# Kernel tuning notes

Hardware: AMD Instinct MI355X
Metric: run time of the kernel (lower is better)

Reference implementation:

```python
import jax, jax.numpy as jnp
import numpy as np

# HGT meta: 2 node types (A=0, B=1), 3 relations (src_type, dst_type)
L, T, R = 3, 2, 3
H, D = 1, 64            # PyG HGTConv default heads=1, head_dim = hidden/heads
F = H * D               # hidden_channels = input feature dim = 64
NA = NB = 131072
E = 1_000_000
REL = [(0, 1), (1, 0), (0, 0)]


def setup_inputs() -> dict:
    key = jax.random.key(0)
    ks = jax.random.split(key, 16)
    sc = 1.0 / np.sqrt(F)
    inp = {}
    inp["xA"] = jax.random.normal(ks[0], (NA, F), jnp.float32)
    inp["xB"] = jax.random.normal(ks[1], (NB, F), jnp.float32)
    # K/Q/V projections per (layer, node_type)
    inp["Wk"] = jax.random.normal(ks[2], (L, T, F, F), jnp.float32) * sc
    inp["bk"] = jnp.zeros((L, T, F), jnp.float32)
    inp["Wq"] = jax.random.normal(ks[3], (L, T, F, F), jnp.float32) * sc
    inp["bq"] = jnp.zeros((L, T, F), jnp.float32)
    inp["Wv"] = jax.random.normal(ks[4], (L, T, F, F), jnp.float32) * sc
    inp["bv"] = jnp.zeros((L, T, F), jnp.float32)
    # per (layer, relation, head) attention / message matrices and priority
    inp["a_rel"] = jax.random.normal(ks[5], (L, R, H, D, D), jnp.float32) * sc
    inp["m_rel"] = jax.random.normal(ks[6], (L, R, H, D, D), jnp.float32) * sc
    inp["p_rel"] = jnp.ones((L, R, H), jnp.float32)
    # output projection + skip gate per (layer, node_type)
    inp["Wa"] = jax.random.normal(ks[7], (L, T, F, F), jnp.float32) * sc
    inp["ba"] = jnp.zeros((L, T, F), jnp.float32)
    inp["skip"] = jnp.ones((L, T), jnp.float32)
    # final readout Linear(hidden, 1)
    inp["lin_w"] = jax.random.normal(ks[8], (F, 1), jnp.float32) * sc
    inp["lin_b"] = jnp.zeros((1,), jnp.float32)
    # edge indices: ei[0]=src, ei[1]=dst (NA == NB so one range works)
    inp["ei1"] = jax.random.randint(ks[9], (2, E), 0, NA, jnp.int32)   # A -> B
    inp["ei2"] = jax.random.randint(ks[10], (2, E), 0, NA, jnp.int32)  # B -> A
    inp["ei3"] = jax.random.randint(ks[11], (2, E), 0, NA, jnp.int32)  # A -> A
    return inp


def _hgt_layer(xs, eis, Wk, bk, Wq, bq, Wv, bv, a_rel, m_rel, p_rel, Wa, ba, skip):
    # per-type K/Q/V projections, reshaped to [N, H, D]
    k = [(xs[t] @ Wk[t] + bk[t]).reshape(-1, H, D) for t in range(T)]
    q = [(xs[t] @ Wq[t] + bq[t]).reshape(-1, H, D) for t in range(T)]
    v = [(xs[t] @ Wv[t] + bv[t]).reshape(-1, H, D) for t in range(T)]
    agg = [jnp.zeros((xs[t].shape[0], H, D), xs[t].dtype) for t in range(T)]
    inv_sqrt_d = jnp.asarray(1.0 / np.sqrt(D), xs[0].dtype)
    for r, (s, d) in enumerate(REL):
        src, dst = eis[r][0], eis[r][1]
        n_d = xs[d].shape[0]
        # relation-specific transforms on source nodes, then edge gather
        k_r = jnp.einsum('nhd,hde->nhe', k[s], a_rel[r])
        v_r = jnp.einsum('nhd,hde->nhe', v[s], m_rel[r])
        # attention score per edge per head: (q_dst . k_src) * p_rel / sqrt(D)
        score = jnp.einsum('ehd,ehd->eh', q[d][dst], k_r[src]) * p_rel[r] * inv_sqrt_d
        # segment softmax over incoming edges of each dst node (per edge type)
        mx = jax.ops.segment_max(score, dst, num_segments=n_d)
        ex = jnp.exp(score - mx[dst])
        den = jax.ops.segment_sum(ex, dst, num_segments=n_d)
        alpha = ex / den[dst]                      # [E, H]
        msg = alpha[:, :, None] * v_r[src]         # [E, H, D]
        agg[d] = agg[d] + jax.ops.segment_sum(msg, dst, num_segments=n_d)
    outs = []
    for t in range(T):
        o = jax.nn.gelu(agg[t].reshape(-1, F), approximate=False) @ Wa[t] + ba[t]
        a = jax.nn.sigmoid(skip[t])               # skip gate (out_dim == in_dim)
        outs.append(a * o + (1.0 - a) * xs[t])
    return outs


def reference(xA, xB, Wk, bk, Wq, bq, Wv, bv, a_rel, m_rel, p_rel, Wa, ba, skip,
              lin_w, lin_b, ei1, ei2, ei3):
    xs = [xA, xB]
    eis = [ei1, ei2, ei3]
    for l in range(L):
        xs = _hgt_layer(xs, eis, Wk[l], bk[l], Wq[l], bq[l], Wv[l], bv[l],
                        a_rel[l], m_rel[l], p_rel[l], Wa[l], ba[l], skip[l])
    x = jnp.concatenate(xs, axis=0)               # concat all node types
    pooled = jnp.sum(x, axis=0, keepdims=True)    # global_add_pool, batch=None
    return pooled @ lin_w + lin_b                 # Linear(hidden, 1) -> [1, 1]
```

## Files before the change

### kernel.cpp

```cpp
#include <hip/hip_runtime.h>
#include <cmath>

#define DEV __device__ __forceinline__

typedef __attribute__((ext_vector_type(8))) short short8v;
typedef __attribute__((ext_vector_type(4))) float f32x4;

DEV float atomicAddF(float* p, float v) {
    return unsafeAtomicAdd(p, v);
}

DEV float gelu_exact(float v) {
    return 0.5f * v * (1.f + erff(v * 0.70710678118654752f));
}

DEV unsigned short f32_to_bf16(float f) {
    union { float f; unsigned int u; } x; x.f = f;
    unsigned int r = x.u + 0x7fffu + ((x.u >> 16) & 1u);
    return (unsigned short)(r >> 16);
}

DEV unsigned int f4_to_fp8x4(float a, float b, float c, float d) {
    int r = __builtin_amdgcn_cvt_pk_fp8_f32(a, b, 0, false);
    r = __builtin_amdgcn_cvt_pk_fp8_f32(c, d, r, true);
    return (unsigned int)r;
}

DEV float4 fp8x4_to_f4(unsigned int w) {
    auto lo = __builtin_amdgcn_cvt_pk_f32_fp8(w, false);
    auto hi = __builtin_amdgcn_cvt_pk_f32_fp8(w, true);
    return make_float4(lo[0], lo[1], hi[0], hi[1]);
}

DEV short8v cvt8_bf16(float4 f0, float4 f1) {
    union { unsigned int u[4]; short8v s; } r;
    asm("v_cvt_pk_bf16_f32 %0, %1, %2" : "=v"(r.u[0]) : "v"(f0.x), "v"(f0.y));
    asm("v_cvt_pk_bf16_f32 %0, %1, %2" : "=v"(r.u[1]) : "v"(f0.z), "v"(f0.w));
    asm("v_cvt_pk_bf16_f32 %0, %1, %2" : "=v"(r.u[2]) : "v"(f1.x), "v"(f1.y));
    asm("v_cvt_pk_bf16_f32 %0, %1, %2" : "=v"(r.u[3]) : "v"(f1.z), "v"(f1.w));
    return r.s;
}


struct MatSetB {
    const unsigned short* Wt[3];
    const float* b[3];
    float*       y[3];
    int          mode[3];
    int          n;
};

#define BCAP2 4608
#define SB_TILE 4096
#define PSTR 129

__global__ __launch_bounds__(256) void combine_w_bf16(
    const float* __restrict__ Wk, const float* __restrict__ bk,
    const float* __restrict__ Wv, const float* __restrict__ bv,
    const float* __restrict__ a_rel, const float* __restrict__ m_rel,
    const float* __restrict__ p_rel, unsigned short* __restrict__ CWt,
    float* __restrict__ Cb)
{
    const int r = blockIdx.x, kv = blockIdx.y, l = blockIdx.z;
    const int srcT[3] = {0, 1, 0};
    const int s = srcT[r];
    const float* Wsrc = (kv == 0 ? Wk : Wv) + ((size_t)(l*2 + s)) * 4096;
    const float* bsrc = (kv == 0 ? bk : bv) + ((size_t)(l*2 + s)) * 64;
    const float* A    = (kv == 0 ? a_rel : m_rel) + ((size_t)(l*3 + r)) * 4096;
    const float scale = (kv == 0) ? p_rel[l*3 + r] * 0.125f : 1.f;

    __shared__ float Ws[4096];
    __shared__ float As[4096];
    const int tid = threadIdx.x;
    for (int k = tid; k < 4096; k += 256) { Ws[k] = Wsrc[k]; As[k] = A[k]; }
    __syncthreads();

    unsigned short* out = CWt + ((size_t)(l*6 + r*2 + kv)) * 4096;
    const int j = tid & 63;
    #pragma unroll
    for (int i = 0; i < 16; i++) {
        const int f = (tid >> 6) * 16 + i;
        float acc = 0.f;
        #pragma unroll
        for (int e = 0; e < 64; e++) acc = fmaf(Ws[f*64 + e], As[e*64 + j], acc);
        const int so = (l == 0) ? f : (4*(f & 15) + (f >> 4));
        out[j*64 + so] = f32_to_bf16(acc * scale);
    }
    if (tid < 64) {
        float acc = 0.f;
        for (int e = 0; e < 64; e++) acc = fmaf(bsrc[e], As[e*64 + tid], acc);
        Cb[(size_t)(l*6 + r*2 + kv) * 64 + tid] = acc * scale;
    }
}

__global__ __launch_bounds__(256) void prep_wt(
    const float* __restrict__ Wq, const float* __restrict__ Wa,
    unsigned short* __restrict__ Wqt, unsigned short* __restrict__ Wat)
{
    const int bid = blockIdx.x;
    const float* src; unsigned short* dst; int useSigma;
    if (bid < 6) { src = Wq + (size_t)bid * 4096; dst = Wqt + (size_t)bid * 4096;
                   useSigma = (bid >= 2); }
    else         { src = Wa + (size_t)(bid - 6) * 4096; dst = Wat + (size_t)(bid - 6) * 4096;
                   useSigma = 1; }
    for (int idx = threadIdx.x; idx < 4096; idx += 256) {
        const int c = idx >> 6, s = idx & 63;
        const int k = useSigma ? (16*(s & 3) + (s >> 2)) : s;
        dst[c*64 + s] = f32_to_bf16(src[k*64 + c]);
    }
}

DEV void proj128_body(const float* __restrict__ x, const MatSetB& ms, int bid, int tid)
{
    const int wv  = tid >> 6;
    const int ln  = tid & 63;
    const int j   = ln & 15;
    const int g   = ln >> 4;
    const long long rowb = (long long)bid * 128 + wv * 32;

    short8v A[2][2];
    #pragma unroll
    for (int rg = 0; rg < 2; rg++) {
        const float* xp = x + (rowb + rg*16 + j) * 64 + g*8;
        #pragma unroll
        for (int ks = 0; ks < 2; ks++) {
            const float4 f0 = *(const float4*)(xp + ks*32);
            const float4 f1 = *(const float4*)(xp + ks*32 + 4);
            A[rg][ks] = cvt8_bf16(f0, f1);
        }
    }

    unsigned int kst[2][4];
    for (int m = 0; m < ms.n; m++) {
        short8v B[4][2];
        #pragma unroll
        for (int ct = 0; ct < 4; ct++) {
            const unsigned short* wp = ms.Wt[m] + (ct*16 + j) * 64 + g*8;
            B[ct][0] = *(const short8v*)(wp);
            B[ct][1] = *(const short8v*)(wp + 32);
        }
        f32x4 acc[2][4];
        #pragma unroll
        for (int ct = 0; ct < 4; ct++) {
            const float bm = ms.b[m][ct*16 + j];
            f32x4 bi = {bm, bm, bm, bm};
            acc[0][ct] = bi; acc[1][ct] = bi;
        }
        #pragma unroll
        for (int rg = 0; rg < 2; rg++)
            #pragma unroll
            for (int ct = 0; ct < 4; ct++) {
                acc[rg][ct] = __builtin_amdgcn_mfma_f32_16x16x32_bf16(
                    A[rg][0], B[ct][0], acc[rg][ct], 0, 0, 0);
                acc[rg][ct] = __builtin_amdgcn_mfma_f32_16x16x32_bf16(
                    A[rg][1], B[ct][1], acc[rg][ct], 0, 0, 0);
            }
        const int mode = ms.mode[m];
        if (mode == 0) {
            float* yb = ms.y[m];
            #pragma unroll
            for (int rg = 0; rg < 2; rg++)
                #pragma unroll
                for (int i = 0; i < 4; i++) {
                    const long long node = rowb + rg*16 + g*4 + i;
                    *(float4*)(yb + node*64 + j*4) = make_float4(
                        acc[rg][0][i], acc[rg][1][i], acc[rg][2][i], acc[rg][3][i]);
                }
        } else if (mode == 1) {
            #pragma unroll
            for (int rg = 0; rg < 2; rg++)
                #pragma unroll
                for (int i = 0; i < 4; i++)
                    kst[rg][i] = f4_to_fp8x4(
                        acc[rg][0][i], acc[rg][1][i], acc[rg][2][i], acc[rg][3][i]);
        } else {
            unsigned char* yb = (unsigned char*)ms.y[m];
            #pragma unroll
            for (int rg = 0; rg < 2; rg++)
                #pragma unroll
                for (int i = 0; i < 4; i++) {
                    const long long node = rowb + rg*16 + g*4 + i;
                    uint2 s;
                    s.x = kst[rg][i];
                    s.y = f4_to_fp8x4(
                        acc[rg][0][i], acc[rg][1][i], acc[rg][2][i], acc[rg][3][i]);
                    *(uint2*)(yb + node*128 + j*8) = s;
                }
        }
    }
}

__global__ __launch_bounds__(256) void proj_triple(
    const float* __restrict__ x1, MatSetB ms1, int g1,
    const float* __restrict__ x2, MatSetB ms2, int g2,
    const float* __restrict__ x3, MatSetB ms3)
{
    const int tid = threadIdx.x;
    int idx = blockIdx.x;
    if (idx < g1) { proj128_body(x1, ms1, idx, tid); return; }
    idx -= g1;
    if (idx < g2) { proj128_body(x2, ms2, idx, tid); return; }
    proj128_body(x3, ms3, idx - g2, tid);
}

struct ScatP { const int* ei; int E; int nbuck; int* bcur; int2* pb; int nblk; };

DEV void scatter_body(const ScatP& sp, int bid, int tid)
{
    __shared__ int  hist[256];
    __shared__ int  lbase[256];
    __shared__ int  gbase[256];
    __shared__ int  lcur[256];
    __shared__ int  scanbuf[256];
    __shared__ int2 stage[SB_TILE];
    const int tile0 = bid * SB_TILE;
    const int E = sp.E;
    const int* ei = sp.ei;

    int2 my[16]; int mb[16];
    #pragma unroll
    for (int i = 0; i < 16; i++) {
        const int e = tile0 + tid + i*256;
        if (e < E) { my[i].x = ei[e]; my[i].y = ei[E + e]; mb[i] = my[i].y >> 9; }
        else mb[i] = -1;
    }
    hist[tid] = 0;
    __syncthreads();
    #pragma unroll
    for (int i = 0; i < 16; i++) if (mb[i] >= 0) atomicAdd(&hist[mb[i]], 1);
    __syncthreads();
    const int c = hist[tid];
    scanbuf[tid] = c;
    __syncthreads();
    for (int off = 1; off < 256; off <<= 1) {
        int add = (tid >= off) ? scanbuf[tid - off] : 0;
        __syncthreads();
        scanbuf[tid] += add;
        __syncthreads();
    }
    lbase[tid] = scanbuf[tid] - c;
    lcur[tid]  = scanbuf[tid] - c;
    if (c > 0 && tid < sp.nbuck) gbase[tid] = atomicAdd(sp.bcur + tid * 16, c);
    __syncthreads();
    #pragma unroll
    for (int i = 0; i < 16; i++) {
        if (mb[i] >= 0) {
            const int p = atomicAdd(&lcur[mb[i]], 1);
            stage[p] = my[i];
        }
    }
    __syncthreads();
    if (c > 0 && tid < sp.nbuck) {
        const int gb = gbase[tid];
        const int lb = lbase[tid];
        int2* dstp = sp.pb + (size_t)tid * BCAP2;
        for (int jj = 0; jj < c; jj++) {
            const int gp = gb + jj;
            if (gp < BCAP2) dstp[gp] = stage[lb + jj];
        }
    }
}

__global__ __launch_bounds__(256) void proj_scatter(
    ScatP s0, ScatP s1, ScatP s2,
    const float* __restrict__ x1, MatSetB ms1, int g1,
    const float* __restrict__ x2, MatSetB ms2, int g2,
    const float* __restrict__ x3, MatSetB ms3)
{
    const int tid = threadIdx.x;
    int idx = blockIdx.x;
    if (idx < s0.nblk) { scatter_body(s0, idx, tid); return; }
    idx -= s0.nblk;
    if (idx < s1.nblk) { scatter_body(s1, idx, tid); return; }
    idx -= s1.nblk;
    if (idx < s2.nblk) { scatter_body(s2, idx, tid); return; }
    idx -= s2.nblk;
    if (idx < g1) { proj128_body(x1, ms1, idx, tid); return; }
    idx -= g1;
    if (idx < g2) { proj128_body(x2, ms2, idx, tid); return; }
    proj128_body(x3, ms3, idx - g2, tid);
}

struct CsrP { const int2* pb; const int* bcur; int* rp; int* re; int* col; int n; int nblk; };

DEV void csr_body(const CsrP& cp, int b, int tid)
{
    __shared__ int lcnt[512];
    __shared__ int lcur[512];
    __shared__ int scanbuf[256];
    int cnt = cp.bcur[b * 16];
    if (cnt > BCAP2) cnt = BCAP2;
    lcnt[tid] = 0; lcnt[tid + 256] = 0;
    __syncthreads();
    const int2* src = cp.pb + (size_t)b * BCAP2;
    for (int i = tid; i < cnt; i += 256)
        atomicAdd(&lcnt[src[i].y & 511], 1);
    __syncthreads();
    const int c0 = lcnt[2*tid], c1 = lcnt[2*tid + 1];
    const int s = c0 + c1;
    scanbuf[tid] = s;
    __syncthreads();
    for (int off = 1; off < 256; off <<= 1) {
        int add = (tid >= off) ? scanbuf[tid - off] : 0;
        __syncthreads();
        scanbuf[tid] += add;
        __syncthreads();
    }
    const int excl = scanbuf[tid] - s;
    const int base = b * BCAP2;
    const int d0 = (b << 9) + 2*tid;
    if (d0 < cp.n)     { cp.rp[d0]   = base + excl;      cp.re[d0]   = base + excl + c0; }
    if (d0 + 1 < cp.n) { cp.rp[d0+1] = base + excl + c0; cp.re[d0+1] = base + excl + c0 + c1; }
    lcur[2*tid] = excl; lcur[2*tid + 1] = excl + c0;
    __syncthreads();
    for (int i = tid; i < cnt; i += 256) {
        const int2 p = src[i];
        const int pos = atomicAdd(&lcur[p.y & 511], 1);
        cp.col[base + pos] = p.x;
    }
}

__global__ __launch_bounds__(256) void csr_all(CsrP c0, CsrP c1, CsrP c2)
{
    const int tid = threadIdx.x;
    int idx = blockIdx.x;
    if (idx < c0.nblk) { csr_body(c0, idx, tid); return; }
    idx -= c0.nblk;
    if (idx < c1.nblk) { csr_body(c1, idx, tid); return; }
    csr_body(c2, idx - c1.nblk, tid);
}

#define PROC_EDGE(KVR)                                                                 \
    {                                                                                  \
        const float4 ka_ = fp8x4_to_f4(KVR.x);                                         \
        const float4 kb2_ = fp8x4_to_f4(KVR.z);                                        \
        float sc_ = q0.x*ka_.x + q0.y*ka_.y + q0.z*ka_.z + q0.w*ka_.w                  \
                  + q1.x*kb2_.x + q1.y*kb2_.y + q1.z*kb2_.z + q1.w*kb2_.w;             \
        sc_ += __shfl_xor(sc_, 1); sc_ += __shfl_xor(sc_, 2); sc_ += __shfl_xor(sc_, 4);\
        const float p_ = __expf(sc_);                                                  \
        const float4 va_ = fp8x4_to_f4(KVR.y);                                         \
        const float4 vb_ = fp8x4_to_f4(KVR.w);                                         \
        ssum_ += p_;                                                                   \
        acc0_.x = fmaf(p_, va_.x, acc0_.x); acc0_.y = fmaf(p_, va_.y, acc0_.y);        \
        acc0_.z = fmaf(p_, va_.z, acc0_.z); acc0_.w = fmaf(p_, va_.w, acc0_.w);        \
        acc1_.x = fmaf(p_, vb_.x, acc1_.x); acc1_.y = fmaf(p_, vb_.y, acc1_.y);        \
        acc1_.z = fmaf(p_, vb_.z, acc1_.z); acc1_.w = fmaf(p_, vb_.w, acc1_.w);        \
    }

#define AGG_BODY(RP, RE, COL, KV, O0, O1)                                              \
    {                                                                                  \
        float4 acc0_ = {0.f,0.f,0.f,0.f}, acc1_ = {0.f,0.f,0.f,0.f};                   \
        float ssum_ = 0.f;                                                             \
        const int ss0_ = (RP)[dst], ss1_ = (RE)[dst];                                  \
        const unsigned char* kb_ = (KV) + sub*16;                                      \
        int e_ = ss0_;                                                                 \
        uint4 qq0_ = {0,0,0,0}, qq1_ = {0,0,0,0}, qq2_ = {0,0,0,0}, qq3_ = {0,0,0,0};  \
        if (e_ < ss1_)     qq0_ = *(const uint4*)(kb_ + (size_t)(COL)[e_] * 128);      \
        if (e_ + 1 < ss1_) qq1_ = *(const uint4*)(kb_ + (size_t)(COL)[e_+1] * 128);    \
        if (e_ + 2 < ss1_) qq2_ = *(const uint4*)(kb_ + (size_t)(COL)[e_+2] * 128);    \
        if (e_ + 3 < ss1_) qq3_ = *(const uint4*)(kb_ + (size_t)(COL)[e_+3] * 128);    \
        for (; e_ + 4 < ss1_; e_ += 2) {                                               \
            const int nn0_ = (COL)[e_+4];                                              \
            const int nn1_ = (e_ + 5 < ss1_) ? (COL)[e_+5] : nn0_;                     \
            const uint4 tt0_ = *(const uint4*)(kb_ + (size_t)nn0_ * 128);              \
            const uint4 tt1_ = *(const uint4*)(kb_ + (size_t)nn1_ * 128);              \
            PROC_EDGE(qq0_)                                                            \
            PROC_EDGE(qq1_)                                                            \
            qq0_ = qq2_; qq1_ = qq3_; qq2_ = tt0_; qq3_ = tt1_;                        \
        }                                                                              \
        if (e_ < ss1_)     PROC_EDGE(qq0_)                                             \
        if (e_ + 1 < ss1_) PROC_EDGE(qq1_)                                             \
        if (e_ + 2 < ss1_) PROC_EDGE(qq2_)                                             \
        if (e_ + 3 < ss1_) PROC_EDGE(qq3_)                                             \
        const float inv_ = (ssum_ > 0.f) ? 1.f / ssum_ : 0.f;                          \
        O0.x = fmaf(acc0_.x, inv_, O0.x); O0.y = fmaf(acc0_.y, inv_, O0.y);            \
        O0.z = fmaf(acc0_.z, inv_, O0.z); O0.w = fmaf(acc0_.w, inv_, O0.w);            \
        O1.x = fmaf(acc1_.x, inv_, O1.x); O1.y = fmaf(acc1_.y, inv_, O1.y);            \
        O1.z = fmaf(acc1_.z, inv_, O1.z); O1.w = fmaf(acc1_.w, inv_, O1.w);            \
    }

DEV void agg_block(
    const int* __restrict__ rp1, const int* __restrict__ re1, const int* __restrict__ c1,
    const int* __restrict__ rp2, const int* __restrict__ re2, const int* __restrict__ c2,
    const float* __restrict__ q,
    const unsigned char* __restrict__ kva, const unsigned char* __restrict__ kvb,
    float* __restrict__ xio, const unsigned short* __restrict__ Wat,
    const float* __restrict__ ba, const float* __restrict__ skipw,
    int xstd, int dual, int dopool, float* __restrict__ vec,
    int bid, int tid, float* lds, float* lds_pool)
{
    const long long rowb = (long long)bid * 128;
    if (tid < 64) lds_pool[tid] = 0.f;

    {
        const int sub = tid & 7;
        const int dl  = tid >> 3;
        const int dst = (int)rowb + dl;
        const float4* qp = (const float4*)(q + (size_t)dst * 64);
        const float4 q0 = qp[sub*2], q1 = qp[sub*2 + 1];
        float4 o0 = {0.f,0.f,0.f,0.f}, o1 = {0.f,0.f,0.f,0.f};
        AGG_BODY(rp1, re1, c1, kva, o0, o1)
        if (dual) {
            AGG_BODY(rp2, re2, c2, kvb, o0, o1)
        }
        float* lp = lds + (size_t)(8*sub) * PSTR + dl;
        lp[0*PSTR] = gelu_exact(o0.x); lp[1*PSTR] = gelu_exact(o0.y);
        lp[2*PSTR] = gelu_exact(o0.z); lp[3*PSTR] = gelu_exact(o0.w);
        lp[4*PSTR] = gelu_exact(o1.x); lp[5*PSTR] = gelu_exact(o1.y);
        lp[6*PSTR] = gelu_exact(o1.z); lp[7*PSTR] = gelu_exact(o1.w);
    }
    __syncthreads();

    if (tid < 512) {
        const int wv = tid >> 6;
        const int ln = tid & 63;
        const int j  = ln & 15;
        const int g  = ln >> 4;
        const int r  = wv*16 + j;

        short8v A[2];
        #pragma unroll
        for (int ks = 0; ks < 2; ks++) {
            const int pb = g*8 + ks*32;
            const float4 f0 = make_float4(lds[(pb+0)*PSTR + r], lds[(pb+1)*PSTR + r],
                                          lds[(pb+2)*PSTR + r], lds[(pb+3)*PSTR + r]);
            const float4 f1 = make_float4(lds[(pb+4)*PSTR + r], lds[(pb+5)*PSTR + r],
                                          lds[(pb+6)*PSTR + r], lds[(pb+7)*PSTR + r]);
            A[ks] = cvt8_bf16(f0, f1);
        }

        f32x4 acc[4];
        #pragma unroll
        for (int ct = 0; ct < 4; ct++) {
            const float bm = ba[ct*16 + j];
            acc[ct] = (f32x4){bm, bm, bm, bm};
        }
        #pragma unroll
        for (int ct = 0; ct < 4; ct++) {
            const unsigned short* wp = Wat + (ct*16 + j) * 64 + g*8;
            const short8v B0 = *(const short8v*)(wp);
            const short8v B1 = *(const short8v*)(wp + 32);
            acc[ct] = __builtin_amdgcn_mfma_f32_16x16x32_bf16(A[0], B0, acc[ct], 0, 0, 0);
            acc[ct] = __builtin_amdgcn_mfma_f32_16x16x32_bf16(A[1], B1, acc[ct], 0, 0, 0);
        }

        const float gate = 1.f / (1.f + __expf(-skipw[0]));
        const float og   = 1.f - gate;
        float4 pacc = {0.f,0.f,0.f,0.f};
        #pragma unroll
        for (int i = 0; i < 4; i++) {
            const long long node = rowb + wv*16 + g*4 + i;
            float* xp = xio + node*64;
            float4 o;
            if (xstd) {
                o.x = gate*acc[0][i] + og*xp[j];
                o.y = gate*acc[1][i] + og*xp[16 + j];
                o.z = gate*acc[2][i] + og*xp[32 + j];
                o.w = gate*acc[3][i] + og*xp[48 + j];
            } else {
                const float4 xo = *(const float4*)(xp + 4*j);
                o = make_float4(gate*acc[0][i] + og*xo.x,
                                gate*acc[1][i] + og*xo.y,
                                gate*acc[2][i] + og*xo.z,
                                gate*acc[3][i] + og*xo.w);
            }
            if (!dopool) {
                *(float4*)(xp + 4*j) = o;
            } else {
                pacc.x += o.x; pacc.y += o.y; pacc.z += o.z; pacc.w += o.w;
            }
        }
        if (dopool) {
            atomicAdd(&lds_pool[4*j + 0], pacc.x);
            atomicAdd(&lds_pool[4*j + 1], pacc.y);
            atomicAdd(&lds_pool[4*j + 2], pacc.z);
            atomicAdd(&lds_pool[4*j + 3], pacc.w);
        }
    }
    __syncthreads();
    if (dopool && tid < 64) atomicAddF(vec + tid, lds_pool[tid]);
}

__global__ __launch_bounds__(1024, 8) void agg_all(
    const int* __restrict__ rp0, const int* __restrict__ re0, const int* __restrict__ c0,
    const float* __restrict__ qB, const unsigned char* __restrict__ kv0,
    float* __restrict__ xB, const unsigned short* __restrict__ WatB,
    const float* __restrict__ baB, const float* __restrict__ skipB,
    const int* __restrict__ rp1, const int* __restrict__ re1, const int* __restrict__ c1,
    const int* __restrict__ rp2, const int* __restrict__ re2, const int* __restrict__ c2,
    const float* __restrict__ qA, const unsigned char* __restrict__ kv1,
    const unsigned char* __restrict__ kv2,
    float* __restrict__ xA, const unsigned short* __restrict__ WatA,
    const float* __restrict__ baA, const float* __restrict__ skipA,
    int xstd, int dopool, float* __restrict__ vec, int aggB, int aggA)
{
    __shared__ float lds[64 * PSTR];
    __shared__ float lds_pool[64];
    const int idx = blockIdx.x;
    const int tid = threadIdx.x;
    const int half = (aggA < aggB) ? aggA : aggB;
    int isDual, bid;
    if (idx < 2*half) { isDual = !(idx & 1); bid = idx >> 1; }
    else              { bid = idx - half;    isDual = (aggA > aggB); }
    if (isDual) {
        agg_block(rp1, re1, c1, rp2, re2, c2, qA, kv1, kv2, xA, WatA, baA, skipA,
                  xstd, 1, dopool, vec, bid, tid, lds, lds_pool);
    } else {
        agg_block(rp0, re0, c0, rp0, re0, c0, qB, kv0, kv0, xB, WatB, baB, skipB,
                  xstd, 0, dopool, vec, bid, tid, lds, lds_pool);
    }
}

__global__ void final_dot(const float* __restrict__ vec, const float* __restrict__ lw,
                          const float* __restrict__ lb, float* __restrict__ out)
{
    const int i = threadIdx.x;
    float v = vec[i] * lw[16*(i & 3) + (i >> 2)];
    #pragma unroll
    for (int m = 32; m >= 1; m >>= 1) v += __shfl_xor(v, m);
    if (i == 0) out[0] = v + lb[0];
}

extern "C" void kernel_launch(void* const* d_in, const int* in_sizes, int n_in,
                              void* d_out, int out_size, void* d_ws, size_t ws_size,
                              hipStream_t stream)
{
    float* xs[2] = {(float*)d_in[0], (float*)d_in[1]};
    const float* Wk    = (const float*)d_in[2];
    const float* bk    = (const float*)d_in[3];
    const float* Wq    = (const float*)d_in[4];
    const float* bq    = (const float*)d_in[5];
    const float* Wv    = (const float*)d_in[6];
    const float* bv    = (const float*)d_in[7];
    const float* a_rel = (const float*)d_in[8];
    const float* m_rel = (const float*)d_in[9];
    const float* p_rel = (const float*)d_in[10];
    const float* Wa    = (const float*)d_in[11];
    const float* ba    = (const float*)d_in[12];
    const float* skipw = (const float*)d_in[13];
    const float* lin_w = (const float*)d_in[14];
    const float* lin_b = (const float*)d_in[15];
    const int*   ei[3] = {(const int*)d_in[16], (const int*)d_in[17], (const int*)d_in[18]};

    const long long NA = in_sizes[0] / 64;
    const long long NB = in_sizes[1] / 64;
    const long long Ns[2] = {NA, NB};
    const long long Nmax = NA > NB ? NA : NB;
    int E[3];
    for (int r = 0; r < 3; r++) E[r] = in_sizes[16 + r] / 2;
    static const int dstN_is_B[3] = {1, 0, 0};
    const long long nbuckMax = (Nmax + 511) >> 9;

    float* w = (float*)d_ws;
    float* qB  = w; w += Nmax * 64;
    float* qA  = w; w += Nmax * 64;
    unsigned char* kv0 = (unsigned char*)w; w += Nmax * 32;
    unsigned char* kv1 = (unsigned char*)w; w += Nmax * 32;
    unsigned char* kv2 = (unsigned char*)w; w += Nmax * 32;
    unsigned short* CWt = (unsigned short*)w; w += 18 * 2048;
    unsigned short* Wqt = (unsigned short*)w; w += 6 * 2048;
    unsigned short* Wat = (unsigned short*)w; w += 6 * 2048;
    float* Cb    = w; w += 18 * 64;
    float* vec   = w; w += 64;
    int* iw = (int*)w;
    int* row_ptr[3]; int* row_end[3]; int* col[3];
    for (int r = 0; r < 3; r++) {
        row_ptr[r] = iw; iw += Nmax;
        row_end[r] = iw; iw += Nmax;
        col[r]     = iw; iw += nbuckMax * BCAP2;
    }
    int* bcur_all = iw; iw += 3 * nbuckMax * 16;
    int2* pb_all  = (int2*)iw;

    combine_w_bf16<<<dim3(3, 2, 3), 256, 0, stream>>>(Wk, bk, Wv, bv, a_rel, m_rel, p_rel, CWt, Cb);
    prep_wt<<<12, 256, 0, stream>>>(Wq, Wa, Wqt, Wat);
    hipMemsetAsync(vec, 0, 64 * sizeof(float), stream);
    hipMemsetAsync(bcur_all, 0, (size_t)3 * nbuckMax * 16 * sizeof(int), stream);

    const int gA = (int)(NA >> 7), gB = (int)(NB >> 7);
    const int aggB = (int)(NB >> 7);
    const int aggA = (int)(NA >> 7);

    MatSetB msB[3], msA[3], msA2[3];
    for (int l = 0; l < 3; l++) {
        msB[l].n = 3;
        msB[l].Wt[0] = Wqt + (size_t)(l*2 + 1) * 4096;  msB[l].b[0] = bq + (size_t)(l*2 + 1) * 64;
        msB[l].y[0] = qB;         msB[l].mode[0] = 0;
        msB[l].Wt[1] = CWt + (size_t)(l*6 + 2) * 4096;  msB[l].b[1] = Cb + (size_t)(l*6 + 2) * 64;
        msB[l].y[1] = nullptr;    msB[l].mode[1] = 1;
        msB[l].Wt[2] = CWt + (size_t)(l*6 + 3) * 4096;  msB[l].b[2] = Cb + (size_t)(l*6 + 3) * 64;
        msB[l].y[2] = (float*)kv1; msB[l].mode[2] = 2;
        msA[l].n = 2;
        msA[l].Wt[0] = CWt + (size_t)(l*6 + 0) * 4096;  msA[l].b[0] = Cb + (size_t)(l*6 + 0) * 64;
        msA[l].y[0] = nullptr;    msA[l].mode[0] = 1;
        msA[l].Wt[1] = CWt + (size_t)(l*6 + 1) * 4096;  msA[l].b[1] = Cb + (size_t)(l*6 + 1) * 64;
        msA[l].y[1] = (float*)kv0; msA[l].mode[1] = 2;
        msA[l].Wt[2] = msA[l].Wt[1]; msA[l].b[2] = msA[l].b[1];
        msA[l].y[2] = msA[l].y[1];  msA[l].mode[2] = 2;
        msA2[l].n = 3;
        msA2[l].Wt[0] = Wqt + (size_t)(l*2 + 0) * 4096;  msA2[l].b[0] = bq + (size_t)(l*2 + 0) * 64;
        msA2[l].y[0] = qA;         msA2[l].mode[0] = 0;
        msA2[l].Wt[1] = CWt + (size_t)(l*6 + 4) * 4096;  msA2[l].b[1] = Cb + (size_t)(l*6 + 4) * 64;
        msA2[l].y[1] = nullptr;    msA2[l].mode[1] = 1;
        msA2[l].Wt[2] = CWt + (size_t)(l*6 + 5) * 4096;  msA2[l].b[2] = Cb + (size_t)(l*6 + 5) * 64;
        msA2[l].y[2] = (float*)kv2; msA2[l].mode[2] = 2;
    }

    ScatP sp[3];
    for (int r = 0; r < 3; r++) {
        sp[r].ei    = ei[r];
        sp[r].E     = E[r];
        sp[r].nbuck = (int)((Ns[dstN_is_B[r]] + 511) >> 9);
        sp[r].bcur  = bcur_all + (size_t)r * nbuckMax * 16;
        sp[r].pb    = pb_all + (size_t)r * nbuckMax * BCAP2;
        sp[r].nblk  = (E[r] + SB_TILE - 1) / SB_TILE;
    }
    proj_scatter<<<sp[0].nblk + sp[1].nblk + sp[2].nblk + gB + gA + gA, 256, 0, stream>>>(
        sp[0], sp[1], sp[2],
        xs[1], msB[0], gB, xs[0], msA[0], gA, xs[0], msA2[0]);

    CsrP cp[3];
    for (int r = 0; r < 3; r++) {
        cp[r].pb   = sp[r].pb;
        cp[r].bcur = sp[r].bcur;
        cp[r].rp   = row_ptr[r];
        cp[r].re   = row_end[r];
        cp[r].col  = col[r];
        cp[r].n    = (int)Ns[dstN_is_B[r]];
        cp[r].nblk = sp[r].nbuck;
    }
    csr_all<<<cp[0].nblk + cp[1].nblk + cp[2].nblk, 256, 0, stream>>>(cp[0], cp[1], cp[2]);

    for (int l = 0; l < 3; l++) {
        const int xstd   = (l == 0) ? 1 : 0;
        const int dopool = (l == 2) ? 1 : 0;
        if (l > 0) {
            proj_triple<<<gB + gA + gA, 256, 0, stream>>>(
                xs[1], msB[l], gB, xs[0], msA[l], gA, xs[0], msA2[l]);
        }
        agg_all<<<aggB + aggA, 1024, 0, stream>>>(
            row_ptr[0], row_end[0], col[0], qB, kv0, xs[1],
            Wat + (size_t)(l*2 + 1) * 4096, ba + (size_t)(l*2 + 1) * 64, skipw + l*2 + 1,
            row_ptr[1], row_end[1], col[1],
            row_ptr[2], row_end[2], col[2],
            qA, kv1, kv2, xs[0],
            Wat + (size_t)(l*2 + 0) * 4096, ba + (size_t)(l*2 + 0) * 64, skipw + l*2 + 0,
            xstd, dopool, vec, aggB, aggA);
    }

    final_dot<<<1, 64, 0, stream>>>(vec, lin_w, lin_b, (float*)d_out);
}
```

Baseline: 762.8 us.

## Fuse next-layer projections into aggregation kernel and store activations in bf16

Removes the separate per-layer proj_triple launch. Each aggregation block now keeps its updated node features in shared memory and immediately computes the next layer's Q/K/V projections with MFMA. K/V buffers are double-buffered across layers so the next layer's outputs do not overwrite data other blocks still read. Q and the intermediate node features are stored as bf16 instead of fp32, which halves their memory traffic but lowers precision. The extra shared memory and work per block may reduce occupancy of the already heavy aggregation kernel.

```diff
diff --git a/kernel.cpp b/kernel.cpp
--- a/kernel.cpp
+++ b/kernel.cpp
@@ -41,6 +41,20 @@
     return r.s;
 }
 
+DEV uint2 f4_to_bf4(float4 v) {
+    uint2 r;
+    asm("v_cvt_pk_bf16_f32 %0, %1, %2" : "=v"(r.x) : "v"(v.x), "v"(v.y));
+    asm("v_cvt_pk_bf16_f32 %0, %1, %2" : "=v"(r.y) : "v"(v.z), "v"(v.w));
+    return r;
+}
+
+DEV float4 bf4_to_f4(uint2 w) {
+    union { unsigned int u; float f; } a, b, c, d;
+    a.u = (w.x & 0xffffu) << 16; b.u =  w.x & 0xffff0000u;
+    c.u = (w.y & 0xffffu) << 16; d.u =  w.y & 0xffff0000u;
+    return make_float4(a.f, b.f, c.f, d.f);
+}
+
 
 struct MatSetB {
     const unsigned short* Wt[3];
@@ -53,6 +67,7 @@
 #define BCAP2 4608
 #define SB_TILE 4096
 #define PSTR 129
+#define XSTR 72
 
 __global__ __launch_bounds__(256) void combine_w_bf16(
     const float* __restrict__ Wk, const float* __restrict__ bk,
@@ -110,7 +125,7 @@
     }
 }
 
-DEV void proj128_body(const float* __restrict__ x, const MatSetB& ms, int bid, int tid)
+DEV void proj128_f32(const float* __restrict__ x, const MatSetB& ms, int bid, int tid)
 {
     const int wv  = tid >> 6;
     const int ln  = tid & 63;
@@ -157,14 +172,14 @@
             }
         const int mode = ms.mode[m];
         if (mode == 0) {
-            float* yb = ms.y[m];
+            unsigned short* yb = (unsigned short*)ms.y[m];
             #pragma unroll
             for (int rg = 0; rg < 2; rg++)
                 #pragma unroll
                 for (int i = 0; i < 4; i++) {
                     const long long node = rowb + rg*16 + g*4 + i;
-                    *(float4*)(yb + node*64 + j*4) = make_float4(
-                        acc[rg][0][i], acc[rg][1][i], acc[rg][2][i], acc[rg][3][i]);
+                    *(uint2*)(yb + node*64 + j*4) = f4_to_bf4(make_float4(
+                        acc[rg][0][i], acc[rg][1][i], acc[rg][2][i], acc[rg][3][i]));
                 }
         } else if (mode == 1) {
             #pragma unroll
@@ -190,17 +205,50 @@
     }
 }
 
-__global__ __launch_bounds__(256) void proj_triple(
-    const float* __restrict__ x1, MatSetB ms1, int g1,
-    const float* __restrict__ x2, MatSetB ms2, int g2,
-    const float* __restrict__ x3, MatSetB ms3)
-{
-    const int tid = threadIdx.x;
-    int idx = blockIdx.x;
-    if (idx < g1) { proj128_body(x1, ms1, idx, tid); return; }
-    idx -= g1;
-    if (idx < g2) { proj128_body(x2, ms2, idx, tid); return; }
-    proj128_body(x3, ms3, idx - g2, tid);
+DEV void run_matsets(short8v A0, short8v A1, const MatSetB& ms, int m0, int m1,
+                     long long rowt, int j, int g)
+{
+    unsigned int kst[4];
+    for (int m = m0; m < m1; m++) {
+        f32x4 acc[4];
+        #pragma unroll
+        for (int ct = 0; ct < 4; ct++) {
+            const float bm = ms.b[m][ct*16 + j];
+            acc[ct] = (f32x4){bm, bm, bm, bm};
+        }
+        #pragma unroll
+        for (int ct = 0; ct < 4; ct++) {
+            const unsigned short* wp = ms.Wt[m] + (ct*16 + j) * 64 + g*8;
+            const short8v B0 = *(const short8v*)(wp);
+            const short8v B1 = *(const short8v*)(wp + 32);
+            acc[ct] = __builtin_amdgcn_mfma_f32_16x16x32_bf16(A0, B0, acc[ct], 0, 0, 0);
+            acc[ct] = __builtin_amdgcn_mfma_f32_16x16x32_bf16(A1, B1, acc[ct], 0, 0, 0);
+        }
+        const int mode = ms.mode[m];
+        if (mode == 0) {
+            unsigned short* yb = (unsigned short*)ms.y[m];
+            #pragma unroll
+            for (int i = 0; i < 4; i++) {
+                const long long node = rowt + g*4 + i;
+                *(uint2*)(yb + node*64 + j*4) = f4_to_bf4(make_float4(
+                    acc[0][i], acc[1][i], acc[2][i], acc[3][i]));
+            }
+        } else if (mode == 1) {
+            #pragma unroll
+            for (int i = 0; i < 4; i++)
+                kst[i] = f4_to_fp8x4(acc[0][i], acc[1][i], acc[2][i], acc[3][i]);
+        } else {
+            unsigned char* yb = (unsigned char*)ms.y[m];
+            #pragma unroll
+            for (int i = 0; i < 4; i++) {
+                const long long node = rowt + g*4 + i;
+                uint2 s;
+                s.x = kst[i];
+                s.y = f4_to_fp8x4(acc[0][i], acc[1][i], acc[2][i], acc[3][i]);
+                *(uint2*)(yb + node*128 + j*8) = s;
+            }
+        }
+    }
 }
 
 struct ScatP { const int* ei; int E; int nbuck; int* bcur; int2* pb; int nblk; };
@@ -275,10 +323,10 @@
     idx -= s1.nblk;
     if (idx < s2.nblk) { scatter_body(s2, idx, tid); return; }
     idx -= s2.nblk;
-    if (idx < g1) { proj128_body(x1, ms1, idx, tid); return; }
+    if (idx < g1) { proj128_f32(x1, ms1, idx, tid); return; }
     idx -= g1;
-    if (idx < g2) { proj128_body(x2, ms2, idx, tid); return; }
-    proj128_body(x3, ms3, idx - g2, tid);
+    if (idx < g2) { proj128_f32(x2, ms2, idx, tid); return; }
+    proj128_f32(x3, ms3, idx - g2, tid);
 }
 
 struct CsrP { const int2* pb; const int* bcur; int* rp; int* re; int* col; int n; int nblk; };
@@ -382,12 +430,13 @@
 DEV void agg_block(
     const int* __restrict__ rp1, const int* __restrict__ re1, const int* __restrict__ c1,
     const int* __restrict__ rp2, const int* __restrict__ re2, const int* __restrict__ c2,
-    const float* __restrict__ q,
+    const unsigned short* __restrict__ q,
     const unsigned char* __restrict__ kva, const unsigned char* __restrict__ kvb,
-    float* __restrict__ xio, const unsigned short* __restrict__ Wat,
+    const float* __restrict__ xf, unsigned short* __restrict__ xw,
+    const unsigned short* __restrict__ Wat,
     const float* __restrict__ ba, const float* __restrict__ skipw,
     int xstd, int dual, int dopool, float* __restrict__ vec,
-    int bid, int tid, float* lds, float* lds_pool)
+    int bid, int tid, float* lds, float* lds_pool, unsigned short* xsh)
 {
     const long long rowb = (long long)bid * 128;
     if (tid < 64) lds_pool[tid] = 0.f;
@@ -396,8 +445,9 @@
         const int sub = tid & 7;
         const int dl  = tid >> 3;
         const int dst = (int)rowb + dl;
-        const float4* qp = (const float4*)(q + (size_t)dst * 64);
-        const float4 q0 = qp[sub*2], q1 = qp[sub*2 + 1];
+        const uint4 qv = *(const uint4*)(q + (size_t)dst * 64 + sub*8);
+        const float4 q0 = bf4_to_f4(make_uint2(qv.x, qv.y));
+        const float4 q1 = bf4_to_f4(make_uint2(qv.z, qv.w));
         float4 o0 = {0.f,0.f,0.f,0.f}, o1 = {0.f,0.f,0.f,0.f};
         AGG_BODY(rp1, re1, c1, kva, o0, o1)
         if (dual) {
@@ -450,22 +500,25 @@
         #pragma unroll
         for (int i = 0; i < 4; i++) {
             const long long node = rowb + wv*16 + g*4 + i;
-            float* xp = xio + node*64;
             float4 o;
             if (xstd) {
+                const float* xp = xf + node*64;
                 o.x = gate*acc[0][i] + og*xp[j];
                 o.y = gate*acc[1][i] + og*xp[16 + j];
                 o.z = gate*acc[2][i] + og*xp[32 + j];
                 o.w = gate*acc[3][i] + og*xp[48 + j];
             } else {
-                const float4 xo = *(const float4*)(xp + 4*j);
+                const float4 xo = bf4_to_f4(*(const uint2*)(xw + node*64 + 4*j));
                 o = make_float4(gate*acc[0][i] + og*xo.x,
                                 gate*acc[1][i] + og*xo.y,
                                 gate*acc[2][i] + og*xo.z,
                                 gate*acc[3][i] + og*xo.w);
             }
             if (!dopool) {
-                *(float4*)(xp + 4*j) = o;
+                const uint2 ob = f4_to_bf4(o);
+                *(uint2*)(xw + node*64 + 4*j) = ob;
+                if (xsh)
+                    *(uint2*)(xsh + (size_t)(wv*16 + g*4 + i) * XSTR + 4*j) = ob;
             } else {
                 pacc.x += o.x; pacc.y += o.y; pacc.z += o.z; pacc.w += o.w;
             }
@@ -483,31 +536,53 @@
 
 __global__ __launch_bounds__(1024, 8) void agg_all(
     const int* __restrict__ rp0, const int* __restrict__ re0, const int* __restrict__ c0,
-    const float* __restrict__ qB, const unsigned char* __restrict__ kv0,
-    float* __restrict__ xB, const unsigned short* __restrict__ WatB,
+    const unsigned short* __restrict__ qB, const unsigned char* __restrict__ kv0,
+    const float* __restrict__ xfB, unsigned short* __restrict__ xwB,
+    const unsigned short* __restrict__ WatB,
     const float* __restrict__ baB, const float* __restrict__ skipB,
     const int* __restrict__ rp1, const int* __restrict__ re1, const int* __restrict__ c1,
     const int* __restrict__ rp2, const int* __restrict__ re2, const int* __restrict__ c2,
-    const float* __restrict__ qA, const unsigned char* __restrict__ kv1,
+    const unsigned short* __restrict__ qA, const unsigned char* __restrict__ kv1,
     const unsigned char* __restrict__ kv2,
-    float* __restrict__ xA, const unsigned short* __restrict__ WatA,
+    const float* __restrict__ xfA, unsigned short* __restrict__ xwA,
+    const unsigned short* __restrict__ WatA,
     const float* __restrict__ baA, const float* __restrict__ skipA,
-    int xstd, int dopool, float* __restrict__ vec, int aggB, int aggA)
+    int xstd, int dopool, float* __restrict__ vec, int aggB, int aggA,
+    int hasNext, MatSetB msBn, MatSetB msAn, MatSetB msA2n)
 {
     __shared__ float lds[64 * PSTR];
     __shared__ float lds_pool[64];
+    __shared__ unsigned short xsh[128 * XSTR];
     const int idx = blockIdx.x;
     const int tid = threadIdx.x;
     const int half = (aggA < aggB) ? aggA : aggB;
     int isDual, bid;
     if (idx < 2*half) { isDual = !(idx & 1); bid = idx >> 1; }
     else              { bid = idx - half;    isDual = (aggA > aggB); }
+    unsigned short* xshp = hasNext ? xsh : nullptr;
     if (isDual) {
-        agg_block(rp1, re1, c1, rp2, re2, c2, qA, kv1, kv2, xA, WatA, baA, skipA,
-                  xstd, 1, dopool, vec, bid, tid, lds, lds_pool);
+        agg_block(rp1, re1, c1, rp2, re2, c2, qA, kv1, kv2, xfA, xwA, WatA, baA, skipA,
+                  xstd, 1, dopool, vec, bid, tid, lds, lds_pool, xshp);
     } else {
-        agg_block(rp0, re0, c0, rp0, re0, c0, qB, kv0, kv0, xB, WatB, baB, skipB,
-                  xstd, 0, dopool, vec, bid, tid, lds, lds_pool);
+        agg_block(rp0, re0, c0, rp0, re0, c0, qB, kv0, kv0, xfB, xwB, WatB, baB, skipB,
+                  xstd, 0, dopool, vec, bid, tid, lds, lds_pool, xshp);
+    }
+    if (!hasNext) return;
+    const int pw  = tid >> 6;
+    const int ln  = tid & 63;
+    const int j   = ln & 15;
+    const int g   = ln >> 4;
+    const int tile = pw & 7;
+    const long long rowt = (long long)bid * 128 + tile * 16;
+    const unsigned short* xr = xsh + (size_t)(tile*16 + j) * XSTR + g*8;
+    const short8v A0 = *(const short8v*)(xr);
+    const short8v A1 = *(const short8v*)(xr + 32);
+    if (isDual) {
+        if (pw < 8) run_matsets(A0, A1, msAn,  0, 2, rowt, j, g);
+        else        run_matsets(A0, A1, msA2n, 0, 3, rowt, j, g);
+    } else {
+        if (pw < 8) run_matsets(A0, A1, msBn, 0, 1, rowt, j, g);
+        else        run_matsets(A0, A1, msBn, 1, 3, rowt, j, g);
     }
 }
 
@@ -552,11 +627,12 @@
     const long long nbuckMax = (Nmax + 511) >> 9;
 
     float* w = (float*)d_ws;
-    float* qB  = w; w += Nmax * 64;
-    float* qA  = w; w += Nmax * 64;
-    unsigned char* kv0 = (unsigned char*)w; w += Nmax * 32;
-    unsigned char* kv1 = (unsigned char*)w; w += Nmax * 32;
-    unsigned char* kv2 = (unsigned char*)w; w += Nmax * 32;
+    unsigned short* qB  = (unsigned short*)w; w += Nmax * 32;
+    unsigned short* qA  = (unsigned short*)w; w += Nmax * 32;
+    unsigned short* xwB = (unsigned short*)w; w += Nmax * 32;
+    unsigned short* xwA = (unsigned short*)w; w += Nmax * 32;
+    unsigned char* kvP0[3];
+    for (int r = 0; r < 3; r++) { kvP0[r] = (unsigned char*)w; w += Nmax * 32; }
     unsigned short* CWt = (unsigned short*)w; w += 18 * 2048;
     unsigned short* Wqt = (unsigned short*)w; w += 6 * 2048;
     unsigned short* Wat = (unsigned short*)w; w += 6 * 2048;
@@ -570,7 +646,11 @@
         col[r]     = iw; iw += nbuckMax * BCAP2;
     }
     int* bcur_all = iw; iw += 3 * nbuckMax * 16;
-    int2* pb_all  = (int2*)iw;
+    int2* pb_all = (int2*)iw;
+    unsigned char* kvP1[3];
+    for (int r = 0; r < 3; r++) kvP1[r] = (unsigned char*)iw + (size_t)r * Nmax * 128;
+
+    unsigned char* kvs[2][3] = {{kvP0[0], kvP0[1], kvP0[2]}, {kvP1[0], kvP1[1], kvP1[2]}};
 
     combine_w_bf16<<<dim3(3, 2, 3), 256, 0, stream>>>(Wk, bk, Wv, bv, a_rel, m_rel, p_rel, CWt, Cb);
     prep_wt<<<12, 256, 0, stream>>>(Wq, Wa, Wqt, Wat);
@@ -583,27 +663,28 @@
 
     MatSetB msB[3], msA[3], msA2[3];
     for (int l = 0; l < 3; l++) {
+        const int p = l & 1;
         msB[l].n = 3;
         msB[l].Wt[0] = Wqt + (size_t)(l*2 + 1) * 4096;  msB[l].b[0] = bq + (size_t)(l*2 + 1) * 64;
-        msB[l].y[0] = qB;         msB[l].mode[0] = 0;
+        msB[l].y[0] = (float*)qB;  msB[l].mode[0] = 0;
         msB[l].Wt[1] = CWt + (size_t)(l*6 + 2) * 4096;  msB[l].b[1] = Cb + (size_t)(l*6 + 2) * 64;
-        msB[l].y[1] = nullptr;    msB[l].mode[1] = 1;
+        msB[l].y[1] = nullptr;     msB[l].mode[1] = 1;
         msB[l].Wt[2] = CWt + (size_t)(l*6 + 3) * 4096;  msB[l].b[2] = Cb + (size_t)(l*6 + 3) * 64;
-        msB[l].y[2] = (float*)kv1; msB[l].mode[2] = 2;
+        msB[l].y[2] = (float*)kvs[p][1]; msB[l].mode[2] = 2;
         msA[l].n = 2;
         msA[l].Wt[0] = CWt + (size_t)(l*6 + 0) * 4096;  msA[l].b[0] = Cb + (size_t)(l*6 + 0) * 64;
-        msA[l].y[0] = nullptr;    msA[l].mode[0] = 1;
+        msA[l].y[0] = nullptr;     msA[l].mode[0] = 1;
         msA[l].Wt[1] = CWt + (size_t)(l*6 + 1) * 4096;  msA[l].b[1] = Cb + (size_t)(l*6 + 1) * 64;
-        msA[l].y[1] = (float*)kv0; msA[l].mode[1] = 2;
+        msA[l].y[1] = (float*)kvs[p][0]; msA[l].mode[1] = 2;
         msA[l].Wt[2] = msA[l].Wt[1]; msA[l].b[2] = msA[l].b[1];
         msA[l].y[2] = msA[l].y[1];  msA[l].mode[2] = 2;
         msA2[l].n = 3;
         msA2[l].Wt[0] = Wqt + (size_t)(l*2 + 0) * 4096;  msA2[l].b[0] = bq + (size_t)(l*2 + 0) * 64;
-        msA2[l].y[0] = qA;         msA2[l].mode[0] = 0;
+        msA2[l].y[0] = (float*)qA;  msA2[l].mode[0] = 0;
         msA2[l].Wt[1] = CWt + (size_t)(l*6 + 4) * 4096;  msA2[l].b[1] = Cb + (size_t)(l*6 + 4) * 64;
-        msA2[l].y[1] = nullptr;    msA2[l].mode[1] = 1;
+        msA2[l].y[1] = nullptr;     msA2[l].mode[1] = 1;
         msA2[l].Wt[2] = CWt + (size_t)(l*6 + 5) * 4096;  msA2[l].b[2] = Cb + (size_t)(l*6 + 5) * 64;
-        msA2[l].y[2] = (float*)kv2; msA2[l].mode[2] = 2;
+        msA2[l].y[2] = (float*)kvs[p][2]; msA2[l].mode[2] = 2;
     }
 
     ScatP sp[3];
@@ -632,20 +713,20 @@
     csr_all<<<cp[0].nblk + cp[1].nblk + cp[2].nblk, 256, 0, stream>>>(cp[0], cp[1], cp[2]);
 
     for (int l = 0; l < 3; l++) {
-        const int xstd   = (l == 0) ? 1 : 0;
-        const int dopool = (l == 2) ? 1 : 0;
-        if (l > 0) {
-            proj_triple<<<gB + gA + gA, 256, 0, stream>>>(
-                xs[1], msB[l], gB, xs[0], msA[l], gA, xs[0], msA2[l]);
-        }
+        const int xstd    = (l == 0) ? 1 : 0;
+        const int dopool  = (l == 2) ? 1 : 0;
+        const int p       = l & 1;
+        const int hasNext = (l < 2) ? 1 : 0;
+        const int nl      = hasNext ? l + 1 : 0;
         agg_all<<<aggB + aggA, 1024, 0, stream>>>(
-            row_ptr[0], row_end[0], col[0], qB, kv0, xs[1],
+            row_ptr[0], row_end[0], col[0], qB, kvs[p][0], xs[1], xwB,
             Wat + (size_t)(l*2 + 1) * 4096, ba + (size_t)(l*2 + 1) * 64, skipw + l*2 + 1,
             row_ptr[1], row_end[1], col[1],
             row_ptr[2], row_end[2], col[2],
-            qA, kv1, kv2, xs[0],
+            qA, kvs[p][1], kvs[p][2], xs[0], xwA,
             Wat + (size_t)(l*2 + 0) * 4096, ba + (size_t)(l*2 + 0) * 64, skipw + l*2 + 0,
-            xstd, dopool, vec, aggB, aggA);
+            xstd, dopool, vec, aggB, aggA,
+            hasNext, msB[nl], msA[nl], msA2[nl]);
     }
 
     final_dot<<<1, 64, 0, stream>>>(vec, lin_w, lin_b, (float*)d_out);
```

Measured after the change: 792.8 us. 3.9% more time.
